# Optimization experiments

Measured on AMD Instinct MI355X. Metric: run time of the kernel, lower is better.

Reference implementation:

```python
import jax, jax.numpy as jnp
import numpy as np

B = 8192
NUM_SAMPLES = 128
RESAMPLE_PADDING = 0.01
F32_EPS = float(np.finfo(np.float32).eps)


def lift_gaussian_diag(d, t_mean, t_var, r_var):
    # d: [B,3]; t_mean/t_var/r_var: [B,S]
    mean = d[..., None, :] * t_mean[..., None]                      # [B,S,3]
    d_mag_sq = jnp.clip(jnp.sum(d ** 2, axis=-1, keepdims=True), 1e-10)
    d_outer_diag = d ** 2
    null_outer_diag = 1.0 - d_outer_diag / d_mag_sq
    cov_diag = (t_var[..., None] * d_outer_diag[..., None, :]
                + r_var[..., None] * null_outer_diag[..., None, :])  # [B,S,3]
    return mean, cov_diag


def conical_frustum_to_gaussian(d, t0, t1, base_radius):
    # stable=True branch of the original code
    mu = (t0 + t1) / 2
    hw = (t1 - t0) / 2
    t_mean = mu + 2 * mu * hw ** 2 / (3 * mu ** 2 + hw ** 2)
    t_var = hw ** 2 / 3 - 4 / 15 * (hw ** 4 * (12 * mu ** 2 - hw ** 2)
                                    / (3 * mu ** 2 + hw ** 2) ** 2)
    r_var = base_radius ** 2 * (mu ** 2 / 4 + 5 / 12 * hw ** 2
                                - 4 / 15 * hw ** 4 / (3 * mu ** 2 + hw ** 2))
    return lift_gaussian_diag(d, t_mean, t_var, r_var)


def cast_rays(t_vals, origins, directions, radii):
    # ray_shape == 'cone', diag == True
    means, covs = conical_frustum_to_gaussian(
        directions, t_vals[..., :-1], t_vals[..., 1:], radii)
    return means + origins[..., None, :], covs


def sorted_piecewise_constant_pdf(bins, weights, num_samples):
    # randomized=False branch; faithful O(n*m) mask-based interval search
    eps = 1e-5
    weight_sum = jnp.sum(weights, axis=-1, keepdims=True)
    padding = jnp.clip(eps - weight_sum, 0)
    weights = weights + padding / weights.shape[-1]
    weight_sum = weight_sum + padding
    pdf = weights / weight_sum
    cdf = jnp.minimum(jnp.cumsum(pdf[..., :-1], axis=-1), 1.0)
    z = jnp.zeros(cdf.shape[:-1] + (1,), cdf.dtype)
    o = jnp.ones(cdf.shape[:-1] + (1,), cdf.dtype)
    cdf = jnp.concatenate([z, cdf, o], axis=-1)                      # [B, nb+1]
    u = jnp.linspace(0.0, 1.0 - F32_EPS, num_samples, dtype=cdf.dtype)
    u = jnp.broadcast_to(u, cdf.shape[:-1] + (num_samples,))         # [B, S]
    mask = u[..., None, :] >= cdf[..., :, None]                      # [B, nb+1, S]

    def find_interval(x):
        x0 = jnp.max(jnp.where(mask, x[..., None], x[..., :1, None]), axis=-2)
        x1 = jnp.min(jnp.where(~mask, x[..., None], x[..., -1:, None]), axis=-2)
        return x0, x1

    bins_g0, bins_g1 = find_interval(bins)
    cdf_g0, cdf_g1 = find_interval(cdf)
    t = jnp.clip(jnp.nan_to_num((u - cdf_g0) / (cdf_g1 - cdf_g0)), 0, 1)
    return bins_g0 + t * (bins_g1 - bins_g0)


def setup_inputs() -> dict:
    key = jax.random.key(0)
    k0, k1, k2, k3 = jax.random.split(key, 4)
    origins = jax.random.normal(k0, (B, 3), dtype=jnp.float32)
    directions = jax.random.normal(k1, (B, 3), dtype=jnp.float32)
    directions = directions / jnp.linalg.norm(directions, axis=-1, keepdims=True)
    radii = 0.001 + 0.01 * jax.random.uniform(k2, (B, 1), dtype=jnp.float32)
    near = 2.0 * jnp.ones((B, 1), dtype=jnp.float32)
    far = 6.0 * jnp.ones((B, 1), dtype=jnp.float32)
    weights = jax.random.uniform(k3, (B, NUM_SAMPLES), dtype=jnp.float32)
    return {"origins": origins, "directions": directions, "radii": radii,
            "near": near, "far": far, "weights": weights}


def reference(origins, directions, radii, near, far, weights):
    # coarse stratified sampling (randomized=False, lindisp=False)
    t = jnp.linspace(0.0, 1.0, NUM_SAMPLES + 1, dtype=jnp.float32)
    t_coarse = near * (1.0 - t) + far * t                            # [B, S+1]
    means_c, covs_c = cast_rays(t_coarse, origins, directions, radii)
    # resample_along_rays: blur weights then inverse-CDF sample
    wpad = jnp.concatenate([weights[..., :1], weights, weights[..., -1:]], axis=-1)
    wmax = jnp.maximum(wpad[..., :-1], wpad[..., 1:])
    wblur = 0.5 * (wmax[..., :-1] + wmax[..., 1:]) + RESAMPLE_PADDING
    t_fine = sorted_piecewise_constant_pdf(t_coarse, wblur, t_coarse.shape[-1])
    means_f, covs_f = cast_rays(t_fine, origins, directions, radii)
    return (t_coarse, means_c, covs_c, t_fine, means_f, covs_f)
```

## Files before the change

kernel.cpp:

```cpp
#include <hip/hip_runtime.h>


constexpr int B_RAYS = 8192;
constexpr int S      = 128;
constexpr int SP1    = 129;
constexpr float F32_EPS = 1.1920928955078125e-07f;
constexpr float USTEP   = (1.0f - F32_EPS) / 128.0f;
constexpr float R_SCALE = 128.0f / (1.0f - F32_EPS);

constexpr long long O_TC = 0;
constexpr long long O_MC = O_TC + (long long)B_RAYS * SP1;
constexpr long long O_CC = O_MC + (long long)B_RAYS * S * 3;
constexpr long long O_TF = O_CC + (long long)B_RAYS * S * 3;
constexpr long long O_MF = O_TF + (long long)B_RAYS * SP1;
constexpr long long O_CF = O_MF + (long long)B_RAYS * S * 3;

typedef float vf4 __attribute__((ext_vector_type(4)));

__device__ __forceinline__ float frcp(float x) { return __builtin_amdgcn_rcpf(x); }

template<int CTRL, int RM>
__device__ __forceinline__ float dpp_addf(float x) {
    int m = __builtin_amdgcn_update_dpp(0, __builtin_bit_cast(int, x),
                                        CTRL, RM, 0xF, true);
    return x + __builtin_bit_cast(float, m);
}
template<int CTRL>
__device__ __forceinline__ float dpp_movf(float x) {
    int m = __builtin_amdgcn_update_dpp(0, __builtin_bit_cast(int, x),
                                        CTRL, 0xF, 0xF, true);
    return __builtin_bit_cast(float, m);
}

__device__ __forceinline__ void st_nt(float* p, float v) {
    __builtin_nontemporal_store(v, p);
}
__device__ __forceinline__ void st_nt4(float* p, float4 v) {
    __builtin_nontemporal_store(__builtin_bit_cast(vf4, v),
                                reinterpret_cast<vf4*>(p));
}

__device__ __forceinline__ void frustum(float t0, float t1, float rad2,
                                        float& tm, float& tv, float& rv)
{
    float mu  = 0.5f * (t0 + t1);
    float hw  = 0.5f * (t1 - t0);
    float mu2 = mu * mu, hw2 = hw * hw, hw4 = hw2 * hw2;
    float den  = fmaf(3.0f, mu2, hw2);
    float rden = frcp(den);
    tm = fmaf(2.0f * mu * hw2, rden, mu);
    tv = hw2 * (1.0f / 3.0f)
       - (4.0f / 15.0f) * (hw4 * fmaf(12.0f, mu2, -hw2)) * (rden * rden);
    rv = rad2 * (0.25f * mu2 + (5.0f / 12.0f) * hw2 - (4.0f / 15.0f) * hw4 * rden);
}

__device__ __forceinline__ float sel3(int c, float x, float y, float z)
{
    return (c == 0) ? x : ((c == 1) ? y : z);
}

__device__ __forceinline__ int smin_of(float c)
{
    int s = (int)ceilf(c * R_SCALE);
    s = s < 0 ? 0 : (s > 129 ? 129 : s);
    #pragma unroll
    for (int it = 0; it < 2; ++it)
        if (s > 0 && (float)(s - 1) * USTEP >= c) --s;
    #pragma unroll
    for (int it = 0; it < 2; ++it)
        if (s < 129 && (float)s * USTEP < c) ++s;
    return s;
}

__global__ __launch_bounds__(256) void mipnerf_kernel(
    const float* __restrict__ origins,
    const float* __restrict__ directions,
    const float* __restrict__ radii,
    const float* __restrict__ nearp,
    const float* __restrict__ farp,
    const float* __restrict__ weights,
    float* __restrict__ out)
{
    const int tid = threadIdx.x;
    const int w   = tid >> 6;
    const int l   = tid & 63;
    const int b   = (blockIdx.x << 2) + w;

    __shared__ float4 s_pay[4][132];

    const float2 wv = *reinterpret_cast<const float2*>(weights + (long long)b * S + 2*l);
    const float ox = origins[3*b+0], oy = origins[3*b+1], oz = origins[3*b+2];
    const float dx = directions[3*b+0], dy = directions[3*b+1], dz = directions[3*b+2];
    const float rad = radii[b];
    const float nv = nearp[b], fv = farp[b];

    const float rad2   = rad * rad;
    const float axx = dx*dx, ayy = dy*dy, azz = dz*dz;
    const float dmag2  = fmaxf(axx + ayy + azz, 1e-10f);
    const float rdmag2 = frcp(dmag2);
    const float nxx = 1.0f - axx * rdmag2;
    const float nyy = 1.0f - ayy * rdmag2;
    const float nzz = 1.0f - azz * rdmag2;

    auto bin = [&](int k) {
        float t = (float)k * (1.0f / 128.0f);
        return nv * (1.0f - t) + fv * t;
    };

    {
        float* ot = out + O_TC + (long long)b * SP1;
        st_nt(ot + l,      bin(l));
        st_nt(ot + l + 64, bin(l + 64));
        if (l == 0) st_nt(ot + 128, bin(128));
    }

    float wprev = dpp_movf<0x138>(wv.y);  if (l == 0)  wprev = wv.x;
    float wnext = dpp_movf<0x130>(wv.x);  if (l == 63) wnext = wv.y;
    float m0 = fmaxf(wprev, wv.x), m1 = fmaxf(wv.x, wv.y), m2 = fmaxf(wv.y, wnext);
    float wb0 = 0.5f * (m0 + m1) + 0.01f;
    float wb1 = 0.5f * (m1 + m2) + 0.01f;

    float ps = wb0 + wb1;
    float x  = ps;
    x = dpp_addf<0x111, 0xF>(x);
    x = dpp_addf<0x112, 0xF>(x);
    x = dpp_addf<0x114, 0xF>(x);
    x = dpp_addf<0x118, 0xF>(x);
    x = dpp_addf<0x142, 0xA>(x);
    x = dpp_addf<0x143, 0xC>(x);
    float incl  = x;
    float total = __builtin_bit_cast(float,
        __builtin_amdgcn_readlane(__builtin_bit_cast(int, incl), 63));

    float pad   = fmaxf(1e-5f - total, 0.0f);
    float wstot = total + pad;
    float inv   = frcp(wstot);
    float padk  = pad * (1.0f / 128.0f);
    float excl  = incl - ps;

    float Av = (l == 0)  ? 0.0f
             : fminf((excl + (float)(2*l) * padk) * inv, 1.0f);
    float Bv = fminf((excl + wb0 + (float)(2*l + 1) * padk) * inv, 1.0f);
    float Cv = (l == 63) ? 1.0f
             : fminf((incl + (float)(2*l + 2) * padk) * inv, 1.0f);

    int sm0 = smin_of(Av);
    int sm1 = smin_of(Bv);
    int sm2 = smin_of(Cv);
    {
        float4 payA = make_float4(Av, Bv - Av, bin(2*l),     bin(2*l + 1));
        float4 payB = make_float4(Bv, Cv - Bv, bin(2*l + 1), bin(2*l + 2));
        for (int s2 = sm0; s2 < sm1; ++s2) s_pay[w][s2] = payA;
        for (int s2 = sm1; s2 < sm2; ++s2) s_pay[w][s2] = payB;
    }
    __builtin_amdgcn_wave_barrier();

    auto emit_span = [&](int m, float t0, float t1, float t2,
                         float* __restrict__ om, float* __restrict__ oc) {
        float tmA, tvA, rvA, tmB, tvB, rvB;
        frustum(t0, t1, rad2, tmA, tvA, rvA);
        frustum(t1, t2, rad2, tmB, tvB, rvB);
        int k0 = m + m / 3;
        int r  = 4*m - 3*k0;
        float4 mv, cv;
        #pragma unroll
        for (int e = 0; e < 4; ++e) {
            int  rc   = r + e;
            bool useB = rc >= 3;
            int  c    = useB ? rc - 3 : rc;
            float tm = useB ? tmB : tmA;
            float tv = useB ? tvB : tvA;
            float rv = useB ? rvB : rvA;
            (&mv.x)[e] = sel3(c, dx, dy, dz) * tm + sel3(c, ox, oy, oz);
            (&cv.x)[e] = tv * sel3(c, axx, ayy, azz) + rv * sel3(c, nxx, nyy, nzz);
        }
        st_nt4(om + 4*m, mv);
        st_nt4(oc + 4*m, cv);
    };

    {
        float* om = out + O_MC + (long long)b * 384;
        float* oc = out + O_CC + (long long)b * 384;
        int k0 = l + l / 3;
        emit_span(l, bin(k0), bin(k0 + 1), bin(k0 + 2), om, oc);
        if (l < 32) {
            int m2s = l + 64;
            int k0b = m2s + m2s / 3;
            emit_span(m2s, bin(k0b), bin(k0b + 1), bin(k0b + 2), om, oc);
        }
    }

    auto tf_of = [&](int s) -> float {
        float4 p = s_pay[w][s];
        float u  = (float)s * USTEP;
        float tt = (u - p.x) * frcp(p.y);
        if (!(tt == tt)) tt = 0.0f;
        tt = fminf(fmaxf(tt, 0.0f), 1.0f);
        return p.z + tt * (p.w - p.z);
    };
    {
        float* ot = out + O_TF + (long long)b * SP1;
        st_nt(ot + l,      tf_of(l));
        st_nt(ot + l + 64, tf_of(l + 64));
        if (l == 0) st_nt(ot + 128, tf_of(128));
    }

    {
        float* om = out + O_MF + (long long)b * 384;
        float* oc = out + O_CF + (long long)b * 384;
        int k0 = l + l / 3;
        emit_span(l, tf_of(k0), tf_of(k0 + 1), tf_of(k0 + 2), om, oc);
        if (l < 32) {
            int m2s = l + 64;
            int k0b = m2s + m2s / 3;
            emit_span(m2s, tf_of(k0b), tf_of(k0b + 1), tf_of(k0b + 2), om, oc);
        }
    }
}

extern "C" void kernel_launch(void* const* d_in, const int* in_sizes, int n_in,
                              void* d_out, int out_size, void* d_ws, size_t ws_size,
                              hipStream_t stream)
{
    const float* origins    = (const float*)d_in[0];
    const float* directions = (const float*)d_in[1];
    const float* radii      = (const float*)d_in[2];
    const float* nearp      = (const float*)d_in[3];
    const float* farp       = (const float*)d_in[4];
    const float* weights    = (const float*)d_in[5];
    float* out = (float*)d_out;

    mipnerf_kernel<<<B_RAYS / 4, 256, 0, stream>>>(
        origins, directions, radii, nearp, farp, weights, out);
}
```

Measured before the change: 18.91 us.

## Split into sampling kernel and flat per-span emit kernel

The single fused kernel is split in two. The first computes coarse bins, the CDF and t_fine, writing t_fine to global memory. The second is launched with one thread per 4-float span across both coarse and fine outputs, reading t_fine back and emitting means and covariances. This spreads the store-heavy emit work evenly over threads, where the old layout left half the lanes idle on the second span. The cost is an extra launch, a global round-trip for t_fine, and redundant per-ray setup in every thread.

```diff
diff --git a/kernel.cpp b/kernel.cpp
--- a/kernel.cpp
+++ b/kernel.cpp
@@ -14,6 +14,9 @@
 constexpr long long O_TF = O_CC + (long long)B_RAYS * S * 3;
 constexpr long long O_MF = O_TF + (long long)B_RAYS * SP1;
 constexpr long long O_CF = O_MF + (long long)B_RAYS * S * 3;
+
+constexpr int SPANS      = 96;
+constexpr int UNITS_CAST = B_RAYS * SPANS;
 
 typedef float vf4 __attribute__((ext_vector_type(4)));
 
@@ -72,10 +75,7 @@
     return s;
 }
 
-__global__ __launch_bounds__(256) void mipnerf_kernel(
-    const float* __restrict__ origins,
-    const float* __restrict__ directions,
-    const float* __restrict__ radii,
+__global__ __launch_bounds__(256) void sample_kernel(
     const float* __restrict__ nearp,
     const float* __restrict__ farp,
     const float* __restrict__ weights,
@@ -89,18 +89,7 @@
     __shared__ float4 s_pay[4][132];
 
     const float2 wv = *reinterpret_cast<const float2*>(weights + (long long)b * S + 2*l);
-    const float ox = origins[3*b+0], oy = origins[3*b+1], oz = origins[3*b+2];
-    const float dx = directions[3*b+0], dy = directions[3*b+1], dz = directions[3*b+2];
-    const float rad = radii[b];
     const float nv = nearp[b], fv = farp[b];
-
-    const float rad2   = rad * rad;
-    const float axx = dx*dx, ayy = dy*dy, azz = dz*dz;
-    const float dmag2  = fmaxf(axx + ayy + azz, 1e-10f);
-    const float rdmag2 = frcp(dmag2);
-    const float nxx = 1.0f - axx * rdmag2;
-    const float nyy = 1.0f - ayy * rdmag2;
-    const float nzz = 1.0f - azz * rdmag2;
 
     auto bin = [&](int k) {
         float t = (float)k * (1.0f / 128.0f);
@@ -154,41 +143,6 @@
         for (int s2 = sm1; s2 < sm2; ++s2) s_pay[w][s2] = payB;
     }
     __builtin_amdgcn_wave_barrier();
-
-    auto emit_span = [&](int m, float t0, float t1, float t2,
-                         float* __restrict__ om, float* __restrict__ oc) {
-        float tmA, tvA, rvA, tmB, tvB, rvB;
-        frustum(t0, t1, rad2, tmA, tvA, rvA);
-        frustum(t1, t2, rad2, tmB, tvB, rvB);
-        int k0 = m + m / 3;
-        int r  = 4*m - 3*k0;
-        float4 mv, cv;
-        #pragma unroll
-        for (int e = 0; e < 4; ++e) {
-            int  rc   = r + e;
-            bool useB = rc >= 3;
-            int  c    = useB ? rc - 3 : rc;
-            float tm = useB ? tmB : tmA;
-            float tv = useB ? tvB : tvA;
-            float rv = useB ? rvB : rvA;
-            (&mv.x)[e] = sel3(c, dx, dy, dz) * tm + sel3(c, ox, oy, oz);
-            (&cv.x)[e] = tv * sel3(c, axx, ayy, azz) + rv * sel3(c, nxx, nyy, nzz);
-        }
-        st_nt4(om + 4*m, mv);
-        st_nt4(oc + 4*m, cv);
-    };
-
-    {
-        float* om = out + O_MC + (long long)b * 384;
-        float* oc = out + O_CC + (long long)b * 384;
-        int k0 = l + l / 3;
-        emit_span(l, bin(k0), bin(k0 + 1), bin(k0 + 2), om, oc);
-        if (l < 32) {
-            int m2s = l + 64;
-            int k0b = m2s + m2s / 3;
-            emit_span(m2s, bin(k0b), bin(k0b + 1), bin(k0b + 2), om, oc);
-        }
-    }
 
     auto tf_of = [&](int s) -> float {
         float4 p = s_pay[w][s];
@@ -204,18 +158,68 @@
         st_nt(ot + l + 64, tf_of(l + 64));
         if (l == 0) st_nt(ot + 128, tf_of(128));
     }
-
-    {
-        float* om = out + O_MF + (long long)b * 384;
-        float* oc = out + O_CF + (long long)b * 384;
-        int k0 = l + l / 3;
-        emit_span(l, tf_of(k0), tf_of(k0 + 1), tf_of(k0 + 2), om, oc);
-        if (l < 32) {
-            int m2s = l + 64;
-            int k0b = m2s + m2s / 3;
-            emit_span(m2s, tf_of(k0b), tf_of(k0b + 1), tf_of(k0b + 2), om, oc);
-        }
-    }
+}
+
+__global__ __launch_bounds__(256) void emit_kernel(
+    const float* __restrict__ origins,
+    const float* __restrict__ directions,
+    const float* __restrict__ radii,
+    const float* __restrict__ nearp,
+    const float* __restrict__ farp,
+    float* out)
+{
+    const int idx  = blockIdx.x * 256 + threadIdx.x;
+    const bool fine = idx >= UNITS_CAST;
+    const int r    = fine ? idx - UNITS_CAST : idx;
+    const int ray  = (int)(((unsigned long long)(unsigned)r * 2863311531ull) >> 38);
+    const int m    = r - ray * SPANS;
+    const int k0   = m + ((m * 43691) >> 17);
+    const int rr   = 4*m - 3*k0;
+
+    float t0, t1, t2;
+    if (fine) {
+        const float* tf = out + O_TF + (long long)ray * SP1;
+        t0 = tf[k0]; t1 = tf[k0 + 1]; t2 = tf[k0 + 2];
+    } else {
+        float nv = nearp[ray], fv = farp[ray];
+        float u0 = (float)k0 * (1.0f / 128.0f);
+        float u1 = (float)(k0 + 1) * (1.0f / 128.0f);
+        float u2 = (float)(k0 + 2) * (1.0f / 128.0f);
+        t0 = nv * (1.0f - u0) + fv * u0;
+        t1 = nv * (1.0f - u1) + fv * u1;
+        t2 = nv * (1.0f - u2) + fv * u2;
+    }
+
+    const float ox = origins[3*ray+0], oy = origins[3*ray+1], oz = origins[3*ray+2];
+    const float dx = directions[3*ray+0], dy = directions[3*ray+1], dz = directions[3*ray+2];
+    const float rad  = radii[ray];
+    const float rad2 = rad * rad;
+    const float axx = dx*dx, ayy = dy*dy, azz = dz*dz;
+    const float dmag2  = fmaxf(axx + ayy + azz, 1e-10f);
+    const float rdmag2 = frcp(dmag2);
+    const float nxx = 1.0f - axx * rdmag2;
+    const float nyy = 1.0f - ayy * rdmag2;
+    const float nzz = 1.0f - azz * rdmag2;
+
+    float tmA, tvA, rvA, tmB, tvB, rvB;
+    frustum(t0, t1, rad2, tmA, tvA, rvA);
+    frustum(t1, t2, rad2, tmB, tvB, rvB);
+
+    float4 mv, cv;
+    #pragma unroll
+    for (int e = 0; e < 4; ++e) {
+        int  rc   = rr + e;
+        bool useB = rc >= 3;
+        int  c    = useB ? rc - 3 : rc;
+        float tm = useB ? tmB : tmA;
+        float tv = useB ? tvB : tvA;
+        float rv = useB ? rvB : rvA;
+        (&mv.x)[e] = sel3(c, dx, dy, dz) * tm + sel3(c, ox, oy, oz);
+        (&cv.x)[e] = tv * sel3(c, axx, ayy, azz) + rv * sel3(c, nxx, nyy, nzz);
+    }
+    const long long fo = 4LL * r;
+    st_nt4(out + (fine ? O_MF : O_MC) + fo, mv);
+    st_nt4(out + (fine ? O_CF : O_CC) + fo, cv);
 }
 
 extern "C" void kernel_launch(void* const* d_in, const int* in_sizes, int n_in,
@@ -230,6 +234,7 @@
     const float* weights    = (const float*)d_in[5];
     float* out = (float*)d_out;
 
-    mipnerf_kernel<<<B_RAYS / 4, 256, 0, stream>>>(
-        origins, directions, radii, nearp, farp, weights, out);
-}
+    sample_kernel<<<B_RAYS / 4, 256, 0, stream>>>(nearp, farp, weights, out);
+    emit_kernel<<<(2 * UNITS_CAST) / 256, 256, 0, stream>>>(
+        origins, directions, radii, nearp, farp, out);
+}
```

Result: slower. 24.00 us (+26.9%).
